# Performance work log

Measured on AMD Instinct MI355X. Metric: run time of the kernel, lower is better.

The kernel has to match this reference:

```python
import jax, jax.numpy as jnp
import numpy as np

N = 1024
NODE_DIM = 3
HIDDEN = 128
NLAYERS = 3
HEADS = 4
HD = HIDDEN // HEADS  # 32
EPS = 1e-5
NEG = -1e9


def setup_inputs() -> dict:
    key = jax.random.key(0)
    ks = jax.random.split(key, 32)
    def w(k, shape, fan_in):
        return jax.random.normal(k, shape, jnp.float32) / np.sqrt(fan_in).astype(np.float32)
    node_features = jax.random.normal(ks[0], (N, NODE_DIM), jnp.float32)
    adj = jax.random.randint(ks[1], (N, N), 0, 2).astype(jnp.float32)
    adj = adj.at[jnp.arange(N), jnp.arange(N)].set(1.0)  # self-loops
    inp = dict(
        node_features=node_features,
        adj=adj,
        Wp=w(ks[2], (NODE_DIM, HIDDEN), NODE_DIM), bp=jnp.zeros((HIDDEN,), jnp.float32),
        Wl=w(ks[3], (NLAYERS, HIDDEN, HIDDEN), HIDDEN),
        Wr=w(ks[4], (NLAYERS, HIDDEN, HIDDEN), HIDDEN),
        Wv=w(ks[5], (NLAYERS, HIDDEN, HIDDEN), HIDDEN),
        att=w(ks[6], (NLAYERS, HD), HD),
        gamma=jnp.ones((NLAYERS, HIDDEN), jnp.float32),
        beta=jnp.zeros((NLAYERS, HIDDEN), jnp.float32),
        Wn1=w(ks[7], (HIDDEN, 64), HIDDEN), bn1=jnp.zeros((64,), jnp.float32),
        Wn2=w(ks[8], (64, 1), 64), bn2=jnp.zeros((1,), jnp.float32),
        Wd1=w(ks[9], (HIDDEN, 64), HIDDEN), bd1=jnp.zeros((64,), jnp.float32),
        Wd2=w(ks[10], (64, 2), 64), bd2=jnp.zeros((2,), jnp.float32),
        Wv1=w(ks[11], (HIDDEN, 64), HIDDEN), bv1=jnp.zeros((64,), jnp.float32),
        Wv2=w(ks[12], (64, 1), 64), bv2=jnp.zeros((1,), jnp.float32),
    )
    return inp


def _gat_layer(h, mask, Wl, Wr, Wv, att, gamma, beta):
    n = h.shape[0]
    wlh = (h @ Wl).reshape(n, HEADS, HD)
    wrh = (h @ Wr).reshape(n, HEADS, HD)
    # pair[i,j,h,d] = LeakyReLU(Wl h_i + Wr h_j)  -- the O(N^2 H D) tensor
    pair = jax.nn.leaky_relu(wlh[:, None, :, :] + wrh[None, :, :, :], 0.2)
    e = jnp.einsum('ijhd,d->ijh', pair, att)
    e = jnp.where(mask[:, :, None], e, NEG)
    alpha = jax.nn.softmax(e, axis=1)  # softmax over neighbours j (dropout = identity in eval)
    v = (h @ Wv).reshape(n, HEADS, HD)
    agg = jnp.einsum('ijh,jhd->ihd', alpha, v).reshape(n, HIDDEN)
    mu = agg.mean(-1, keepdims=True)
    var = agg.var(-1, keepdims=True)
    out = (agg - mu) / jnp.sqrt(var + EPS) * gamma + beta
    return jax.nn.relu(out)


def reference(node_features, adj, Wp, bp, Wl, Wr, Wv, att, gamma, beta,
              Wn1, bn1, Wn2, bn2, Wd1, bd1, Wd2, bd2, Wv1, bv1, Wv2, bv2):
    mask = adj > 0.5
    h = jax.nn.relu(node_features @ Wp + bp)
    for l in range(NLAYERS):
        h = h + _gat_layer(h, mask, Wl[l], Wr[l], Wv[l], att[l], gamma[l], beta[l])
    node_logits = (jax.nn.relu(h @ Wn1 + bn1) @ Wn2 + bn2).squeeze(-1)
    delta_mu = jax.nn.relu(h @ Wd1 + bd1) @ Wd2 + bd2
    pooled = h.mean(axis=0)
    value = (jax.nn.relu(pooled @ Wv1 + bv1) @ Wv2 + bv2).squeeze(-1)
    return (node_logits, delta_mu, value)
```

## Files before the change

kernel.cpp:

```cpp
#include <hip/hip_runtime.h>
#include <hip/hip_bf16.h>

#define NN 1024
#define HID 128
#define NHEADS 4
#define HDD 32
#define NL 3

constexpr int OFF_CONV = 16;
constexpr int OFF_NF   = OFF_CONV;
constexpr int OFF_WP   = OFF_NF  + 3072;
constexpr int OFF_BP   = OFF_WP  + 384;
constexpr int OFF_WL   = OFF_BP  + 128;
constexpr int OFF_WR   = OFF_WL  + 49152;
constexpr int OFF_WVW  = OFF_WR  + 49152;
constexpr int OFF_ATT  = OFF_WVW + 49152;
constexpr int OFF_GAM  = OFF_ATT + 96;
constexpr int OFF_BET  = OFF_GAM + 384;
constexpr int OFF_WN1  = OFF_BET + 384;
constexpr int OFF_BN1  = OFF_WN1 + 8192;
constexpr int OFF_WN2  = OFF_BN1 + 64;
constexpr int OFF_BN2  = OFF_WN2 + 64;
constexpr int OFF_WD1  = OFF_BN2 + 1;
constexpr int OFF_BD1  = OFF_WD1 + 8192;
constexpr int OFF_WD2  = OFF_BD1 + 64;
constexpr int OFF_BD2  = OFF_WD2 + 128;
constexpr int OFF_WV1  = OFF_BD2 + 2;
constexpr int OFF_BV1  = OFF_WV1 + 8192;
constexpr int OFF_WV2  = OFF_BV1 + 64;
constexpr int OFF_BV2  = OFF_WV2 + 64;
constexpr int OFF_CONV_END = OFF_BV2 + 1;
constexpr int CONV_TOTAL = OFF_CONV_END - OFF_CONV;
constexpr int OFF_MASK = 176960;
constexpr int OFF_H    = OFF_MASK + NN*32;
constexpr int OFF_WLH  = OFF_H   + NN*HID;
constexpr int OFF_WRH  = OFF_WLH + NN*HID;
constexpr int OFF_WVH  = OFF_WRH + NN*HID;
constexpr int OFF_CL   = OFF_WVH + NN*HID;
constexpr int OFF_CR   = OFF_CL  + NHEADS*NN;

__device__ __forceinline__ float bf2f(unsigned short u) {
    return __uint_as_float(((unsigned)u) << 16);
}
__device__ __forceinline__ void store_out(void* out, int idx, float v, bool bf) {
    if (bf) {
        unsigned u = __float_as_uint(v);
        unsigned r = (u + 0x7FFFu + ((u >> 16) & 1u)) >> 16;
        ((unsigned short*)out)[idx] = (unsigned short)r;
    } else {
        ((float*)out)[idx] = v;
    }
}
__device__ __forceinline__ bool detect_bf(const unsigned* nf) {
    unsigned w = nf[threadIdx.x & 63];
    int e = (int)((w >> 23) & 0xFFu);
    unsigned long long b = __ballot(e >= 110 && e <= 140);
    return __popcll(b) < 32;
}

struct P21 { const void* p[21]; };
__device__ const int g_sizes[21] = {3072,384,128,49152,49152,49152,96,384,384,
                                    8192,64,64,1,8192,64,128,2,8192,64,64,1};
__device__ const int g_dsts[21] = {OFF_NF,OFF_WP,OFF_BP,OFF_WL,OFF_WR,OFF_WVW,OFF_ATT,
                                   OFF_GAM,OFF_BET,OFF_WN1,OFF_BN1,OFF_WN2,OFF_BN2,
                                   OFF_WD1,OFF_BD1,OFF_WD2,OFF_BD2,OFF_WV1,OFF_BV1,
                                   OFF_WV2,OFF_BV2};
__global__ __launch_bounds__(256) void k_convert(P21 in, const unsigned* nf, float* ws) {
    bool bf = detect_bf(nf);
    int g = blockIdx.x * blockDim.x + threadIdx.x;
    if (g >= CONV_TOTAL) return;
    int rem = g, s = 0;
    while (s < 21 && rem >= g_sizes[s]) { rem -= g_sizes[s]; s++; }
    if (s >= 21) return;
    float v;
    if (bf) v = bf2f(((const unsigned short*)in.p[s])[rem]);
    else    v = ((const float*)in.p[s])[rem];
    ws[g_dsts[s] + rem] = v;
}

__global__ __launch_bounds__(1024) void k_mask(const void* adj, const unsigned* nf, float* ws) {
    bool bf = detect_bf(nf);
    unsigned* mask = (unsigned*)(ws + OFF_MASK);
    int i = blockIdx.x, t = threadIdx.x;
    float v = bf ? bf2f(((const unsigned short*)adj)[i * NN + t])
                 : ((const float*)adj)[i * NN + t];
    unsigned long long b = __ballot(v > 0.5f);
    int lane = t & 63, wv = t >> 6;
    if (lane == 0) {
        mask[i * 32 + wv * 2]     = (unsigned)b;
        mask[i * 32 + wv * 2 + 1] = (unsigned)(b >> 32);
    }
}

__global__ __launch_bounds__(128) void k_h0(float* ws) {
    int i = blockIdx.x, c = threadIdx.x;
    const float* nf = ws + OFF_NF;
    const float* Wp = ws + OFF_WP;
    float a = ws[OFF_BP + c];
    #pragma unroll
    for (int k = 0; k < 3; k++) a += nf[i * 3 + k] * Wp[k * HID + c];
    ws[OFF_H + i * HID + c] = fmaxf(a, 0.0f);
}

__global__ __launch_bounds__(128) void k_mm3(float* ws, int l) {
    __shared__ float hs[4][HID];
    int c = threadIdx.x, i0 = blockIdx.x * 4, which = blockIdx.y;
    const float* h = ws + OFF_H;
    #pragma unroll
    for (int r = 0; r < 4; r++) hs[r][c] = h[(i0 + r) * HID + c];
    __syncthreads();
    int woff = (which == 0) ? OFF_WL : (which == 1) ? OFF_WR : OFF_WVW;
    const float* W = ws + woff + l * HID * HID;
    float a[4] = {0,0,0,0};
    #pragma unroll 4
    for (int k = 0; k < HID; k++) {
        float w = W[k * HID + c];
        #pragma unroll
        for (int r = 0; r < 4; r++) a[r] += hs[r][k] * w;
    }
    if (which == 0) {
        #pragma unroll
        for (int r = 0; r < 4; r++) ws[OFF_WLH + (i0 + r) * HID + c] = a[r];
        float att = ws[OFF_ATT + l * HDD + (c & 31)];
        #pragma unroll
        for (int r = 0; r < 4; r++) {
            float t = att * a[r];
            #pragma unroll
            for (int off = 1; off < 32; off <<= 1) t += __shfl_xor(t, off, 64);
            if ((c & 31) == 0) ws[OFF_CL + (c >> 5) * NN + (i0 + r)] = 0.6f * t;
        }
    } else {
        int doff = (which == 1) ? OFF_WRH : OFF_WVH;
        #pragma unroll
        for (int r = 0; r < 4; r++)
            ws[doff + (c >> 2) * (NN * 4) + (i0 + r) * 4 + (c & 3)] = a[r];
        if (which == 1) {
            float att = ws[OFF_ATT + l * HDD + (c & 31)];
            #pragma unroll
            for (int r = 0; r < 4; r++) {
                float t = att * a[r];
                #pragma unroll
                for (int off = 1; off < 32; off <<= 1) t += __shfl_xor(t, off, 64);
                if ((c & 31) == 0) ws[OFF_CR + (c >> 5) * NN + (i0 + r)] = 0.6f * t;
            }
        }
    }
}

__global__ __launch_bounds__(256) void k_attn(float* ws, int l) {
    int i = blockIdx.x, t = threadIdx.x;
    int lane = t & 63;
    int h = __builtin_amdgcn_readfirstlane(t >> 6);
    __shared__ unsigned mrow[32];
    __shared__ float buf[4][64][33];
    __shared__ float invs[4];
    __shared__ float agg_s[HID];
    __shared__ float red[4];
    const unsigned* mask = (const unsigned*)(ws + OFF_MASK);
    if (t < 32) mrow[t] = mask[i * 32 + t];
    __syncthreads();

    unsigned mbits = 0;
    #pragma unroll
    for (int jc = 0; jc < 16; jc++)
        mbits |= ((mrow[jc * 2 + (lane >> 5)] >> (lane & 31)) & 1u) << jc;

    float att_r[32], wl_r[32];
    const float* attp = ws + OFF_ATT + l * HDD;
    const float* wlp  = ws + OFF_WLH + i * HID + h * HDD;
    #pragma unroll
    for (int d = 0; d < 32; d++) { att_r[d] = 0.4f * attp[d]; wl_r[d] = wlp[d]; }
    float cl6 = ws[OFF_CL + h * NN + i];

    const float* wrT = ws + OFF_WRH + h * 8 * (NN * 4) + lane * 4;
    const float* wvT = ws + OFF_WVH + h * 8 * (NN * 4) + lane * 4;
    const float* crp = ws + OFF_CR + h * NN;

    float m = -1e30f;
    #pragma unroll 1
    for (int jc = 0; jc < 16; jc++) {
        float cr6 = crp[jc * 64 + lane];
        float dot = 0.0f;
        #pragma unroll
        for (int dq = 0; dq < 8; dq++) {
            float4 w = *(const float4*)(wrT + dq * (NN * 4) + jc * 256);
            dot = fmaf(att_r[dq*4+0], fabsf(wl_r[dq*4+0] + w.x), dot);
            dot = fmaf(att_r[dq*4+1], fabsf(wl_r[dq*4+1] + w.y), dot);
            dot = fmaf(att_r[dq*4+2], fabsf(wl_r[dq*4+2] + w.z), dot);
            dot = fmaf(att_r[dq*4+3], fabsf(wl_r[dq*4+3] + w.w), dot);
        }
        float ej = (cl6 + cr6) + dot;
        ej = ((mbits >> jc) & 1u) ? ej : -1e9f;
        buf[h][lane][jc] = ej;
        m = fmaxf(m, ej);
    }
    #pragma unroll
    for (int off = 32; off > 0; off >>= 1) m = fmaxf(m, __shfl_xor(m, off, 64));

    float acc[32];
    #pragma unroll
    for (int d = 0; d < 32; d++) acc[d] = 0.0f;
    float lsum = 0.0f;
    #pragma unroll 1
    for (int jc = 0; jc < 16; jc++) {
        float pe = __expf(buf[h][lane][jc] - m);
        lsum += pe;
        #pragma unroll
        for (int dq = 0; dq < 8; dq++) {
            float4 v = *(const float4*)(wvT + dq * (NN * 4) + jc * 256);
            acc[dq*4+0] = fmaf(pe, v.x, acc[dq*4+0]);
            acc[dq*4+1] = fmaf(pe, v.y, acc[dq*4+1]);
            acc[dq*4+2] = fmaf(pe, v.z, acc[dq*4+2]);
            acc[dq*4+3] = fmaf(pe, v.w, acc[dq*4+3]);
        }
    }
    #pragma unroll
    for (int off = 32; off > 0; off >>= 1) lsum += __shfl_xor(lsum, off, 64);
    if (lane == 0) invs[h] = 1.0f / lsum;
    #pragma unroll
    for (int d = 0; d < 32; d++) buf[h][lane][d] = acc[d];
    __syncthreads();

    {
        int h2 = t >> 6, idx = t & 63, d = idx & 31, half = idx >> 5;
        float s = 0.0f;
        #pragma unroll
        for (int lq = 0; lq < 32; lq++) s += buf[h2][half * 32 + lq][d];
        s += __shfl_xor(s, 32, 64);
        if (half == 0) agg_s[h2 * 32 + d] = s * invs[h2];
    }
    __syncthreads();

    float s = 0.f, s2 = 0.f, agg = 0.f;
    if (t < HID) {
        agg = agg_s[t];
        s = agg; s2 = agg * agg;
        #pragma unroll
        for (int off = 32; off > 0; off >>= 1) {
            s  += __shfl_xor(s,  off, 64);
            s2 += __shfl_xor(s2, off, 64);
        }
        if ((t & 63) == 0) { red[(t >> 6) * 2] = s; red[(t >> 6) * 2 + 1] = s2; }
    }
    __syncthreads();
    if (t < HID) {
        float ts = red[0] + red[2], ts2 = red[1] + red[3];
        float mu  = ts  * (1.0f / HID);
        float var = ts2 * (1.0f / HID) - mu * mu;
        float g  = ws[OFF_GAM + l * HID + t];
        float be = ws[OFF_BET + l * HID + t];
        float o = (agg - mu) * rsqrtf(var + 1e-5f) * g + be;
        ws[OFF_H + i * HID + t] += fmaxf(o, 0.0f);
    }
}

__global__ __launch_bounds__(64) void k_heads(float* ws, const unsigned* nf, void* out) {
    bool bf = detect_bf(nf);
    int i = blockIdx.x, t = threadIdx.x;
    __shared__ float hrow[HID];
    hrow[t]      = ws[OFF_H + i * HID + t];
    hrow[t + 64] = ws[OFF_H + i * HID + t + 64];
    __syncthreads();
    const float* Wn1 = ws + OFF_WN1;
    const float* Wd1 = ws + OFF_WD1;
    float z1 = ws[OFF_BN1 + t], zd = ws[OFF_BD1 + t];
    #pragma unroll 4
    for (int k = 0; k < HID; k++) {
        float hk = hrow[k];
        z1 += hk * Wn1[k * 64 + t];
        zd += hk * Wd1[k * 64 + t];
    }
    z1 = fmaxf(z1, 0.0f); zd = fmaxf(zd, 0.0f);
    float lg = z1 * ws[OFF_WN2 + t];
    float d0 = zd * ws[OFF_WD2 + t * 2 + 0];
    float d1 = zd * ws[OFF_WD2 + t * 2 + 1];
    #pragma unroll
    for (int off = 32; off > 0; off >>= 1) {
        lg += __shfl_xor(lg, off, 64);
        d0 += __shfl_xor(d0, off, 64);
        d1 += __shfl_xor(d1, off, 64);
    }
    if (t == 0) {
        store_out(out, i,              lg + ws[OFF_BN2],     bf);
        store_out(out, NN + i * 2 + 0, d0 + ws[OFF_BD2 + 0], bf);
        store_out(out, NN + i * 2 + 1, d1 + ws[OFF_BD2 + 1], bf);
    }
}

__global__ __launch_bounds__(1024) void k_value(float* ws, const unsigned* nf, void* out) {
    bool bf = detect_bf(nf);
    __shared__ float part[8 * HID];
    __shared__ float pooled[HID];
    int t = threadIdx.x;
    int g = t >> 7, c = t & 127;
    float s = 0.0f;
    for (int r = 0; r < 128; r++) s += ws[OFF_H + (g * 128 + r) * HID + c];
    part[g * HID + c] = s;
    __syncthreads();
    if (t < HID) {
        float p = 0.0f;
        #pragma unroll
        for (int gg = 0; gg < 8; gg++) p += part[gg * HID + t];
        pooled[t] = p * (1.0f / NN);
    }
    __syncthreads();
    if (t < 64) {
        float z = ws[OFF_BV1 + t];
        for (int k = 0; k < HID; k++) z += pooled[k] * ws[OFF_WV1 + k * 64 + t];
        z = fmaxf(z, 0.0f);
        float pv = z * ws[OFF_WV2 + t];
        #pragma unroll
        for (int off = 32; off > 0; off >>= 1) pv += __shfl_xor(pv, off, 64);
        if (t == 0) store_out(out, 3072, pv + ws[OFF_BV2], bf);
    }
}

extern "C" void kernel_launch(void* const* d_in, const int* in_sizes, int n_in,
                              void* d_out, int out_size, void* d_ws, size_t ws_size,
                              hipStream_t stream) {
    float* ws = (float*)d_ws;
    const unsigned* nf = (const unsigned*)d_in[0];

    P21 ptrs;
    const int map[21] = {0,2,3,4,5,6,7,8,9,10,11,12,13,14,15,16,17,18,19,20,21};
    for (int s = 0; s < 21; s++) ptrs.p[s] = d_in[map[s]];
    k_convert<<<(CONV_TOTAL + 255) / 256, 256, 0, stream>>>(ptrs, nf, ws);

    k_mask<<<NN, 1024, 0, stream>>>(d_in[1], nf, ws);
    k_h0<<<NN, 128, 0, stream>>>(ws);

    for (int l = 0; l < NL; l++) {
        k_mm3<<<dim3(NN / 4, 3), 128, 0, stream>>>(ws, l);
        k_attn<<<NN, 256, 0, stream>>>(ws, l);
    }

    k_heads<<<NN, 64, 0, stream>>>(ws, nf, d_out);
    k_value<<<1, 1024, 0, stream>>>(ws, nf, d_out);
}
```

Before: 278.9 us.

## Process two query nodes per wave in attention and fuse pre/post kernels

The attention kernel now has each wave handle two query rows (iA, iB) per head, with 4 nodes per 512-thread block. Each loaded Wr/Wv float4 is reused for two rows, halving global/L2 traffic per node. The preprocessing kernels (convert, mask, h0) are merged into one launch, and the head/value kernels into another, to cut launch overhead. The cost is doubled accumulator register pressure (accA/accB) and extra LDS reduction phases, which may lower occupancy.

```diff
diff --git a/kernel.cpp b/kernel.cpp
--- a/kernel.cpp
+++ b/kernel.cpp
@@ -31,6 +31,7 @@
 constexpr int OFF_BV2  = OFF_WV2 + 64;
 constexpr int OFF_CONV_END = OFF_BV2 + 1;
 constexpr int CONV_TOTAL = OFF_CONV_END - OFF_CONV;
+constexpr int CB = (CONV_TOTAL + 255) / 256;
 constexpr int OFF_MASK = 176960;
 constexpr int OFF_H    = OFF_MASK + NN*32;
 constexpr int OFF_WLH  = OFF_H   + NN*HID;
@@ -51,6 +52,9 @@
         ((float*)out)[idx] = v;
     }
 }
+__device__ __forceinline__ float ldraw(const void* p, int idx, bool bf) {
+    return bf ? bf2f(((const unsigned short*)p)[idx]) : ((const float*)p)[idx];
+}
 __device__ __forceinline__ bool detect_bf(const unsigned* nf) {
     unsigned w = nf[threadIdx.x & 63];
     int e = (int)((w >> 23) & 0xFFu);
@@ -65,41 +69,41 @@
                                    OFF_GAM,OFF_BET,OFF_WN1,OFF_BN1,OFF_WN2,OFF_BN2,
                                    OFF_WD1,OFF_BD1,OFF_WD2,OFF_BD2,OFF_WV1,OFF_BV1,
                                    OFF_WV2,OFF_BV2};
-__global__ __launch_bounds__(256) void k_convert(P21 in, const unsigned* nf, float* ws) {
+
+__global__ __launch_bounds__(256) void k_pre(P21 in, const void* adj, const unsigned* nf, float* ws) {
     bool bf = detect_bf(nf);
-    int g = blockIdx.x * blockDim.x + threadIdx.x;
-    if (g >= CONV_TOTAL) return;
-    int rem = g, s = 0;
-    while (s < 21 && rem >= g_sizes[s]) { rem -= g_sizes[s]; s++; }
-    if (s >= 21) return;
-    float v;
-    if (bf) v = bf2f(((const unsigned short*)in.p[s])[rem]);
-    else    v = ((const float*)in.p[s])[rem];
-    ws[g_dsts[s] + rem] = v;
-}
-
-__global__ __launch_bounds__(1024) void k_mask(const void* adj, const unsigned* nf, float* ws) {
-    bool bf = detect_bf(nf);
-    unsigned* mask = (unsigned*)(ws + OFF_MASK);
-    int i = blockIdx.x, t = threadIdx.x;
-    float v = bf ? bf2f(((const unsigned short*)adj)[i * NN + t])
-                 : ((const float*)adj)[i * NN + t];
-    unsigned long long b = __ballot(v > 0.5f);
-    int lane = t & 63, wv = t >> 6;
-    if (lane == 0) {
-        mask[i * 32 + wv * 2]     = (unsigned)b;
-        mask[i * 32 + wv * 2 + 1] = (unsigned)(b >> 32);
-    }
-}
-
-__global__ __launch_bounds__(128) void k_h0(float* ws) {
-    int i = blockIdx.x, c = threadIdx.x;
-    const float* nf = ws + OFF_NF;
-    const float* Wp = ws + OFF_WP;
-    float a = ws[OFF_BP + c];
-    #pragma unroll
-    for (int k = 0; k < 3; k++) a += nf[i * 3 + k] * Wp[k * HID + c];
-    ws[OFF_H + i * HID + c] = fmaxf(a, 0.0f);
+    int b = blockIdx.x, t = threadIdx.x;
+    if (b < CB) {
+        int g = b * 256 + t;
+        if (g >= CONV_TOTAL) return;
+        int rem = g, s = 0;
+        while (s < 21 && rem >= g_sizes[s]) { rem -= g_sizes[s]; s++; }
+        if (s >= 21) return;
+        ws[g_dsts[s] + rem] = ldraw(in.p[s], rem, bf);
+    } else if (b < CB + NN) {
+        int i = b - CB;
+        unsigned* mask = (unsigned*)(ws + OFF_MASK);
+        int lane = t & 63, wv = t >> 6;
+        #pragma unroll
+        for (int q = 0; q < 4; q++) {
+            int seg = wv * 4 + q;
+            int j = seg * 64 + lane;
+            float v = ldraw(adj, i * NN + j, bf);
+            unsigned long long bl = __ballot(v > 0.5f);
+            if (lane == 0) {
+                mask[i * 32 + seg * 2]     = (unsigned)bl;
+                mask[i * 32 + seg * 2 + 1] = (unsigned)(bl >> 32);
+            }
+        }
+    } else {
+        int bb = b - CB - NN;
+        int i = bb * 2 + (t >> 7), c = t & 127;
+        float a = ldraw(in.p[2], c, bf);
+        #pragma unroll
+        for (int k = 0; k < 3; k++)
+            a += ldraw(in.p[0], i * 3 + k, bf) * ldraw(in.p[1], k * HID + c, bf);
+        ws[OFF_H + i * HID + c] = fmaxf(a, 0.0f);
+    }
 }
 
 __global__ __launch_bounds__(128) void k_mm3(float* ws, int l) {
@@ -147,171 +151,219 @@
     }
 }
 
-__global__ __launch_bounds__(256) void k_attn(float* ws, int l) {
-    int i = blockIdx.x, t = threadIdx.x;
+__global__ __launch_bounds__(512) void k_attn(float* ws, int l) {
+    int t = threadIdx.x;
+    int i0 = blockIdx.x * 4;
     int lane = t & 63;
-    int h = __builtin_amdgcn_readfirstlane(t >> 6);
-    __shared__ unsigned mrow[32];
-    __shared__ float buf[4][64][33];
-    __shared__ float invs[4];
-    __shared__ float agg_s[HID];
-    __shared__ float red[4];
-    const unsigned* mask = (const unsigned*)(ws + OFF_MASK);
-    if (t < 32) mrow[t] = mask[i * 32 + t];
+    int w = t >> 6;
+    int h = __builtin_amdgcn_readfirstlane(w & 3);
+    int p = __builtin_amdgcn_readfirstlane(w >> 2);
+    int iA = i0 + 2 * p, iB = iA + 1;
+
+    __shared__ unsigned mrow[4][32];
+    __shared__ float ebuf[8][64][33];
+    __shared__ float invs[4][4];
+    __shared__ float agg_s[4][HID];
+    __shared__ float red2[4][2][2];
+
+    if (t < 128) mrow[t >> 5][t & 31] = ((const unsigned*)(ws + OFF_MASK))[i0 * 32 + t];
     __syncthreads();
 
-    unsigned mbits = 0;
-    #pragma unroll
-    for (int jc = 0; jc < 16; jc++)
-        mbits |= ((mrow[jc * 2 + (lane >> 5)] >> (lane & 31)) & 1u) << jc;
-
-    float att_r[32], wl_r[32];
+    unsigned mbA = 0, mbB = 0;
+    #pragma unroll
+    for (int jc = 0; jc < 16; jc++) {
+        int wi = jc * 2 + (lane >> 5);
+        mbA |= ((mrow[2 * p][wi] >> (lane & 31)) & 1u) << jc;
+        mbB |= ((mrow[2 * p + 1][wi] >> (lane & 31)) & 1u) << jc;
+    }
+
+    float att_r[32], wlA[32], wlB[32];
     const float* attp = ws + OFF_ATT + l * HDD;
-    const float* wlp  = ws + OFF_WLH + i * HID + h * HDD;
-    #pragma unroll
-    for (int d = 0; d < 32; d++) { att_r[d] = 0.4f * attp[d]; wl_r[d] = wlp[d]; }
-    float cl6 = ws[OFF_CL + h * NN + i];
+    const float* wlpA = ws + OFF_WLH + iA * HID + h * HDD;
+    const float* wlpB = ws + OFF_WLH + iB * HID + h * HDD;
+    #pragma unroll
+    for (int d = 0; d < 32; d++) {
+        att_r[d] = 0.4f * attp[d];
+        wlA[d] = wlpA[d];
+        wlB[d] = wlpB[d];
+    }
+    float clA = ws[OFF_CL + h * NN + iA];
+    float clB = ws[OFF_CL + h * NN + iB];
 
     const float* wrT = ws + OFF_WRH + h * 8 * (NN * 4) + lane * 4;
     const float* wvT = ws + OFF_WVH + h * 8 * (NN * 4) + lane * 4;
     const float* crp = ws + OFF_CR + h * NN;
 
-    float m = -1e30f;
+    float mA = -1e30f, mB = -1e30f;
     #pragma unroll 1
     for (int jc = 0; jc < 16; jc++) {
         float cr6 = crp[jc * 64 + lane];
-        float dot = 0.0f;
+        float dA = 0.0f, dB = 0.0f;
         #pragma unroll
         for (int dq = 0; dq < 8; dq++) {
-            float4 w = *(const float4*)(wrT + dq * (NN * 4) + jc * 256);
-            dot = fmaf(att_r[dq*4+0], fabsf(wl_r[dq*4+0] + w.x), dot);
-            dot = fmaf(att_r[dq*4+1], fabsf(wl_r[dq*4+1] + w.y), dot);
-            dot = fmaf(att_r[dq*4+2], fabsf(wl_r[dq*4+2] + w.z), dot);
-            dot = fmaf(att_r[dq*4+3], fabsf(wl_r[dq*4+3] + w.w), dot);
-        }
-        float ej = (cl6 + cr6) + dot;
-        ej = ((mbits >> jc) & 1u) ? ej : -1e9f;
-        buf[h][lane][jc] = ej;
-        m = fmaxf(m, ej);
-    }
-    #pragma unroll
-    for (int off = 32; off > 0; off >>= 1) m = fmaxf(m, __shfl_xor(m, off, 64));
-
-    float acc[32];
-    #pragma unroll
-    for (int d = 0; d < 32; d++) acc[d] = 0.0f;
-    float lsum = 0.0f;
+            float4 wv4 = *(const float4*)(wrT + dq * (NN * 4) + jc * 256);
+            dA = fmaf(att_r[dq*4+0], fabsf(wlA[dq*4+0] + wv4.x), dA);
+            dB = fmaf(att_r[dq*4+0], fabsf(wlB[dq*4+0] + wv4.x), dB);
+            dA = fmaf(att_r[dq*4+1], fabsf(wlA[dq*4+1] + wv4.y), dA);
+            dB = fmaf(att_r[dq*4+1], fabsf(wlB[dq*4+1] + wv4.y), dB);
+            dA = fmaf(att_r[dq*4+2], fabsf(wlA[dq*4+2] + wv4.z), dA);
+            dB = fmaf(att_r[dq*4+2], fabsf(wlB[dq*4+2] + wv4.z), dB);
+            dA = fmaf(att_r[dq*4+3], fabsf(wlA[dq*4+3] + wv4.w), dA);
+            dB = fmaf(att_r[dq*4+3], fabsf(wlB[dq*4+3] + wv4.w), dB);
+        }
+        float eA = (clA + cr6) + dA; eA = ((mbA >> jc) & 1u) ? eA : -1e9f;
+        float eB = (clB + cr6) + dB; eB = ((mbB >> jc) & 1u) ? eB : -1e9f;
+        ebuf[w][lane][jc]      = eA;
+        ebuf[w][lane][16 + jc] = eB;
+        mA = fmaxf(mA, eA);
+        mB = fmaxf(mB, eB);
+    }
+    #pragma unroll
+    for (int off = 32; off > 0; off >>= 1) {
+        mA = fmaxf(mA, __shfl_xor(mA, off, 64));
+        mB = fmaxf(mB, __shfl_xor(mB, off, 64));
+    }
+
+    float accA[32], accB[32];
+    #pragma unroll
+    for (int d = 0; d < 32; d++) { accA[d] = 0.0f; accB[d] = 0.0f; }
+    float lsA = 0.0f, lsB = 0.0f;
     #pragma unroll 1
     for (int jc = 0; jc < 16; jc++) {
-        float pe = __expf(buf[h][lane][jc] - m);
-        lsum += pe;
+        float peA = __expf(ebuf[w][lane][jc]      - mA);
+        float peB = __expf(ebuf[w][lane][16 + jc] - mB);
+        lsA += peA; lsB += peB;
         #pragma unroll
         for (int dq = 0; dq < 8; dq++) {
-            float4 v = *(const float4*)(wvT + dq * (NN * 4) + jc * 256);
-            acc[dq*4+0] = fmaf(pe, v.x, acc[dq*4+0]);
-            acc[dq*4+1] = fmaf(pe, v.y, acc[dq*4+1]);
-            acc[dq*4+2] = fmaf(pe, v.z, acc[dq*4+2]);
-            acc[dq*4+3] = fmaf(pe, v.w, acc[dq*4+3]);
-        }
-    }
-    #pragma unroll
-    for (int off = 32; off > 0; off >>= 1) lsum += __shfl_xor(lsum, off, 64);
-    if (lane == 0) invs[h] = 1.0f / lsum;
-    #pragma unroll
-    for (int d = 0; d < 32; d++) buf[h][lane][d] = acc[d];
+            float4 v4 = *(const float4*)(wvT + dq * (NN * 4) + jc * 256);
+            accA[dq*4+0] = fmaf(peA, v4.x, accA[dq*4+0]);
+            accB[dq*4+0] = fmaf(peB, v4.x, accB[dq*4+0]);
+            accA[dq*4+1] = fmaf(peA, v4.y, accA[dq*4+1]);
+            accB[dq*4+1] = fmaf(peB, v4.y, accB[dq*4+1]);
+            accA[dq*4+2] = fmaf(peA, v4.z, accA[dq*4+2]);
+            accB[dq*4+2] = fmaf(peB, v4.z, accB[dq*4+2]);
+            accA[dq*4+3] = fmaf(peA, v4.w, accA[dq*4+3]);
+            accB[dq*4+3] = fmaf(peB, v4.w, accB[dq*4+3]);
+        }
+    }
+    #pragma unroll
+    for (int off = 32; off > 0; off >>= 1) {
+        lsA += __shfl_xor(lsA, off, 64);
+        lsB += __shfl_xor(lsB, off, 64);
+    }
+    if (lane == 0) {
+        invs[2 * p][h]     = 1.0f / lsA;
+        invs[2 * p + 1][h] = 1.0f / lsB;
+    }
     __syncthreads();
 
+    float* rbuf = &ebuf[0][0][0];
     {
-        int h2 = t >> 6, idx = t & 63, d = idx & 31, half = idx >> 5;
+        int reg = p * 4 + h;
+        #pragma unroll
+        for (int d = 0; d < 32; d++) rbuf[(reg * 64 + lane) * 33 + d] = accA[d];
+        __syncthreads();
+        int g = t >> 6, d = lane & 31, half = lane >> 5;
         float s = 0.0f;
         #pragma unroll
-        for (int lq = 0; lq < 32; lq++) s += buf[h2][half * 32 + lq][d];
+        for (int lq = 0; lq < 32; lq++) s += rbuf[(g * 64 + half * 32 + lq) * 33 + d];
         s += __shfl_xor(s, 32, 64);
-        if (half == 0) agg_s[h2 * 32 + d] = s * invs[h2];
-    }
-    __syncthreads();
-
-    float s = 0.f, s2 = 0.f, agg = 0.f;
-    if (t < HID) {
-        agg = agg_s[t];
-        s = agg; s2 = agg * agg;
+        int node = 2 * (g >> 2), hh = g & 3;
+        if (half == 0) agg_s[node][hh * 32 + d] = s * invs[node][hh];
+        __syncthreads();
+    }
+    {
+        int reg = p * 4 + h;
+        #pragma unroll
+        for (int d = 0; d < 32; d++) rbuf[(reg * 64 + lane) * 33 + d] = accB[d];
+        __syncthreads();
+        int g = t >> 6, d = lane & 31, half = lane >> 5;
+        float s = 0.0f;
+        #pragma unroll
+        for (int lq = 0; lq < 32; lq++) s += rbuf[(g * 64 + half * 32 + lq) * 33 + d];
+        s += __shfl_xor(s, 32, 64);
+        int node = 2 * (g >> 2) + 1, hh = g & 3;
+        if (half == 0) agg_s[node][hh * 32 + d] = s * invs[node][hh];
+        __syncthreads();
+    }
+
+    {
+        int n = t >> 7, f = t & 127;
+        float agg = agg_s[n][f];
+        float s = agg, s2 = agg * agg;
         #pragma unroll
         for (int off = 32; off > 0; off >>= 1) {
             s  += __shfl_xor(s,  off, 64);
             s2 += __shfl_xor(s2, off, 64);
         }
-        if ((t & 63) == 0) { red[(t >> 6) * 2] = s; red[(t >> 6) * 2 + 1] = s2; }
-    }
-    __syncthreads();
-    if (t < HID) {
-        float ts = red[0] + red[2], ts2 = red[1] + red[3];
+        int half = (t >> 6) & 1;
+        if (lane == 0) { red2[n][half][0] = s; red2[n][half][1] = s2; }
+        __syncthreads();
+        float ts  = red2[n][0][0] + red2[n][1][0];
+        float ts2 = red2[n][0][1] + red2[n][1][1];
         float mu  = ts  * (1.0f / HID);
         float var = ts2 * (1.0f / HID) - mu * mu;
-        float g  = ws[OFF_GAM + l * HID + t];
-        float be = ws[OFF_BET + l * HID + t];
-        float o = (agg - mu) * rsqrtf(var + 1e-5f) * g + be;
-        ws[OFF_H + i * HID + t] += fmaxf(o, 0.0f);
-    }
-}
-
-__global__ __launch_bounds__(64) void k_heads(float* ws, const unsigned* nf, void* out) {
+        float gm = ws[OFF_GAM + l * HID + f];
+        float be = ws[OFF_BET + l * HID + f];
+        float o = (agg - mu) * rsqrtf(var + 1e-5f) * gm + be;
+        ws[OFF_H + (i0 + n) * HID + f] += fmaxf(o, 0.0f);
+    }
+}
+
+__global__ __launch_bounds__(256) void k_post(float* ws, const unsigned* nf, void* out) {
     bool bf = detect_bf(nf);
-    int i = blockIdx.x, t = threadIdx.x;
-    __shared__ float hrow[HID];
-    hrow[t]      = ws[OFF_H + i * HID + t];
-    hrow[t + 64] = ws[OFF_H + i * HID + t + 64];
-    __syncthreads();
-    const float* Wn1 = ws + OFF_WN1;
-    const float* Wd1 = ws + OFF_WD1;
-    float z1 = ws[OFF_BN1 + t], zd = ws[OFF_BD1 + t];
-    #pragma unroll 4
-    for (int k = 0; k < HID; k++) {
-        float hk = hrow[k];
-        z1 += hk * Wn1[k * 64 + t];
-        zd += hk * Wd1[k * 64 + t];
-    }
-    z1 = fmaxf(z1, 0.0f); zd = fmaxf(zd, 0.0f);
-    float lg = z1 * ws[OFF_WN2 + t];
-    float d0 = zd * ws[OFF_WD2 + t * 2 + 0];
-    float d1 = zd * ws[OFF_WD2 + t * 2 + 1];
-    #pragma unroll
-    for (int off = 32; off > 0; off >>= 1) {
-        lg += __shfl_xor(lg, off, 64);
-        d0 += __shfl_xor(d0, off, 64);
-        d1 += __shfl_xor(d1, off, 64);
-    }
-    if (t == 0) {
-        store_out(out, i,              lg + ws[OFF_BN2],     bf);
-        store_out(out, NN + i * 2 + 0, d0 + ws[OFF_BD2 + 0], bf);
-        store_out(out, NN + i * 2 + 1, d1 + ws[OFF_BD2 + 1], bf);
-    }
-}
-
-__global__ __launch_bounds__(1024) void k_value(float* ws, const unsigned* nf, void* out) {
-    bool bf = detect_bf(nf);
-    __shared__ float part[8 * HID];
-    __shared__ float pooled[HID];
-    int t = threadIdx.x;
-    int g = t >> 7, c = t & 127;
-    float s = 0.0f;
-    for (int r = 0; r < 128; r++) s += ws[OFF_H + (g * 128 + r) * HID + c];
-    part[g * HID + c] = s;
-    __syncthreads();
-    if (t < HID) {
-        float p = 0.0f;
-        #pragma unroll
-        for (int gg = 0; gg < 8; gg++) p += part[gg * HID + t];
-        pooled[t] = p * (1.0f / NN);
-    }
-    __syncthreads();
-    if (t < 64) {
-        float z = ws[OFF_BV1 + t];
-        for (int k = 0; k < HID; k++) z += pooled[k] * ws[OFF_WV1 + k * 64 + t];
-        z = fmaxf(z, 0.0f);
-        float pv = z * ws[OFF_WV2 + t];
-        #pragma unroll
-        for (int off = 32; off > 0; off >>= 1) pv += __shfl_xor(pv, off, 64);
-        if (t == 0) store_out(out, 3072, pv + ws[OFF_BV2], bf);
+    int b = blockIdx.x, t = threadIdx.x;
+    if (b < 256) {
+        __shared__ float hrow[4][HID];
+        int n = t >> 6, tt = t & 63;
+        int i = b * 4 + n;
+        hrow[n][tt]      = ws[OFF_H + i * HID + tt];
+        hrow[n][tt + 64] = ws[OFF_H + i * HID + tt + 64];
+        __syncthreads();
+        const float* Wn1 = ws + OFF_WN1;
+        const float* Wd1 = ws + OFF_WD1;
+        float z1 = ws[OFF_BN1 + tt], zd = ws[OFF_BD1 + tt];
+        #pragma unroll 4
+        for (int k = 0; k < HID; k++) {
+            float hk = hrow[n][k];
+            z1 += hk * Wn1[k * 64 + tt];
+            zd += hk * Wd1[k * 64 + tt];
+        }
+        z1 = fmaxf(z1, 0.0f); zd = fmaxf(zd, 0.0f);
+        float lg = z1 * ws[OFF_WN2 + tt];
+        float d0 = zd * ws[OFF_WD2 + tt * 2 + 0];
+        float d1 = zd * ws[OFF_WD2 + tt * 2 + 1];
+        #pragma unroll
+        for (int off = 32; off > 0; off >>= 1) {
+            lg += __shfl_xor(lg, off, 64);
+            d0 += __shfl_xor(d0, off, 64);
+            d1 += __shfl_xor(d1, off, 64);
+        }
+        if (tt == 0) {
+            store_out(out, i,              lg + ws[OFF_BN2],     bf);
+            store_out(out, NN + i * 2 + 0, d0 + ws[OFF_BD2 + 0], bf);
+            store_out(out, NN + i * 2 + 1, d1 + ws[OFF_BD2 + 1], bf);
+        }
+    } else {
+        __shared__ float part[2][HID];
+        __shared__ float pooled[HID];
+        int g = t >> 7, c = t & 127;
+        float s = 0.0f;
+        #pragma unroll 4
+        for (int r = g; r < NN; r += 2) s += ws[OFF_H + r * HID + c];
+        part[g][c] = s;
+        __syncthreads();
+        if (t < HID) pooled[t] = (part[0][t] + part[1][t]) * (1.0f / NN);
+        __syncthreads();
+        if (t < 64) {
+            float z = ws[OFF_BV1 + t];
+            for (int k = 0; k < HID; k++) z += pooled[k] * ws[OFF_WV1 + k * 64 + t];
+            z = fmaxf(z, 0.0f);
+            float pv = z * ws[OFF_WV2 + t];
+            #pragma unroll
+            for (int off = 32; off > 0; off >>= 1) pv += __shfl_xor(pv, off, 64);
+            if (t == 0) store_out(out, 3072, pv + ws[OFF_BV2], bf);
+        }
     }
 }
 
@@ -324,16 +376,13 @@
     P21 ptrs;
     const int map[21] = {0,2,3,4,5,6,7,8,9,10,11,12,13,14,15,16,17,18,19,20,21};
     for (int s = 0; s < 21; s++) ptrs.p[s] = d_in[map[s]];
-    k_convert<<<(CONV_TOTAL + 255) / 256, 256, 0, stream>>>(ptrs, nf, ws);
-
-    k_mask<<<NN, 1024, 0, stream>>>(d_in[1], nf, ws);
-    k_h0<<<NN, 128, 0, stream>>>(ws);
+
+    k_pre<<<CB + NN + NN / 2, 256, 0, stream>>>(ptrs, d_in[1], nf, ws);
 
     for (int l = 0; l < NL; l++) {
         k_mm3<<<dim3(NN / 4, 3), 128, 0, stream>>>(ws, l);
-        k_attn<<<NN, 256, 0, stream>>>(ws, l);
-    }
-
-    k_heads<<<NN, 64, 0, stream>>>(ws, nf, d_out);
-    k_value<<<1, 1024, 0, stream>>>(ws, nf, d_out);
-}
+        k_attn<<<NN / 4, 512, 0, stream>>>(ws, l);
+    }
+
+    k_post<<<257, 256, 0, stream>>>(ws, nf, d_out);
+}
```

Measured after the change: 255.6 us. 8.3% less time.
